# Optimization experiments

Hardware: AMD Instinct MI355X
Metric: run time of the kernel (lower is better)

Reference implementation:

```python
import jax, jax.numpy as jnp
import numpy as np

DIM = 512
HEADS = 8
HEAD_DIM = DIM // HEADS
SCALING = float(np.sqrt(HEAD_DIM))
B, S = 8, 2048


def setup_inputs() -> dict:
    key = jax.random.key(0)
    ks = jax.random.split(key, 6)
    x = jax.random.normal(ks[0], (B, S, DIM), dtype=jnp.float32)
    mask = jax.random.randint(ks[1], (B, S), 0, 2).astype(bool)
    mask = mask.at[:, 0].set(False)  # guarantee at least one unmasked key per row
    lim_qkv = 1.0 / np.sqrt(DIM)
    Wqkv = jax.random.uniform(ks[2], (3 * DIM, DIM), minval=-lim_qkv, maxval=lim_qkv, dtype=jnp.float32)
    bqkv = jax.random.uniform(ks[3], (3 * DIM,), minval=-lim_qkv, maxval=lim_qkv, dtype=jnp.float32)
    Wout = jax.random.uniform(ks[4], (DIM, DIM), minval=-lim_qkv, maxval=lim_qkv, dtype=jnp.float32)
    bout = jax.random.uniform(ks[5], (DIM,), minval=-lim_qkv, maxval=lim_qkv, dtype=jnp.float32)
    ln_g = jnp.ones((DIM,), dtype=jnp.float32)
    ln_b = jnp.zeros((DIM,), dtype=jnp.float32)
    return {"x": x, "mask": mask, "Wqkv": Wqkv, "bqkv": bqkv, "Wout": Wout, "bout": bout, "ln_g": ln_g, "ln_b": ln_b}


def reference(x, mask, Wqkv, bqkv, Wout, bout, ln_g, ln_b):
    b, s, _ = x.shape
    qkv = x @ Wqkv.T + bqkv                                   # [b, s, 3*dim]
    qkv = qkv.reshape(b, s, HEADS, HEAD_DIM, 3)               # torch reshape semantics (interleaved)
    q = qkv[..., 0]                                           # [b, s, h, d]
    k = qkv[..., 1]
    v = jax.nn.elu(qkv[..., 2])
    attn = jnp.einsum('bqhd,bkhd->bhqk', q, k) / SCALING      # [b, h, s, s]
    bias = jnp.where(mask[:, None, None, :], -jnp.inf, 0.0).astype(attn.dtype)
    attn = jax.nn.softmax(attn + bias, axis=-1)
    out = jnp.einsum('bhqk,bkhd->bqhd', attn, v).reshape(b, s, DIM)
    out = out @ Wout.T + bout
    mu = jnp.mean(out, axis=-1, keepdims=True)
    var = jnp.var(out, axis=-1, keepdims=True)
    out = (out - mu) / jnp.sqrt(var + 1e-5) * ln_g + ln_b
    return jax.nn.elu(out)
```

## Files before the change

kernel.cpp:

```cpp
#include <hip/hip_runtime.h>

#define DIM 512
#define HEADS 8
#define HD 64
#define NB 8
#define NS 2048
#define SCALE_INV 0.125f
#define NEG_BIG -1e30f
#define QSZ 8388608

typedef __attribute__((ext_vector_type(8))) short bf16x8;
typedef __attribute__((ext_vector_type(4))) float f32x4;

__device__ __forceinline__ float elu_f(float x) {
    return x > 0.0f ? x : (__expf(x) - 1.0f);
}
__device__ __forceinline__ short f2bf(float x) {
    union { float f; unsigned u; } v; v.f = x;
    unsigned r = v.u + 0x7FFFu + ((v.u >> 16) & 1u);
    return (short)(r >> 16);
}
__device__ __forceinline__ unsigned pack_bf_t(float a, float b) {
    union { float f; unsigned u; } va, vb; va.f = a; vb.f = b;
    return (va.u >> 16) | (vb.u & 0xFFFF0000u);
}

__device__ __forceinline__ void gload16(const void* g, void* l) {
    __builtin_amdgcn_global_load_lds(
        (const __attribute__((address_space(1))) unsigned*)g,
        (__attribute__((address_space(3))) unsigned*)l, 16, 0, 0);
}
__device__ __forceinline__ void gload4(const void* g, void* l) {
    __builtin_amdgcn_global_load_lds(
        (const __attribute__((address_space(1))) unsigned*)g,
        (__attribute__((address_space(3))) unsigned*)l, 4, 0, 0);
}

#define X4 2097152
#define W14 196608
#define W24 65536
__global__ __launch_bounds__(256) void prep(
    const float* __restrict__ x, const float* __restrict__ Wqkv,
    const float* __restrict__ bqkv, const float* __restrict__ Wout,
    const int* __restrict__ mask,
    short* __restrict__ xb, short* __restrict__ Wp,
    float* __restrict__ bp, short* __restrict__ Wob,
    float* __restrict__ maskf)
{
    int i = blockIdx.x * 256 + threadIdx.x;
    if (i < X4) {
        float4 v = *(const float4*)(x + (size_t)i * 4);
        ushort4 o; o.x = (unsigned short)f2bf(v.x); o.y = (unsigned short)f2bf(v.y);
        o.z = (unsigned short)f2bf(v.z); o.w = (unsigned short)f2bf(v.w);
        *(ushort4*)(xb + (size_t)i * 4) = o;
    } else if (i < X4 + W14) {
        int j = i - X4;
        int np = j >> 7, k = (j & 127) * 4;
        int w = np >> 9, h = (np >> 6) & 7, d = np & 63;
        int n = h * 192 + d * 3 + w;
        float4 v = *(const float4*)(Wqkv + (size_t)n * 512 + k);
        ushort4 o; o.x = (unsigned short)f2bf(v.x); o.y = (unsigned short)f2bf(v.y);
        o.z = (unsigned short)f2bf(v.z); o.w = (unsigned short)f2bf(v.w);
        *(ushort4*)(Wp + (size_t)np * 512 + k) = o;
    } else if (i < X4 + W14 + W24) {
        int j = i - X4 - W14;
        float4 v = *(const float4*)(Wout + (size_t)j * 4);
        ushort4 o; o.x = (unsigned short)f2bf(v.x); o.y = (unsigned short)f2bf(v.y);
        o.z = (unsigned short)f2bf(v.z); o.w = (unsigned short)f2bf(v.w);
        *(ushort4*)(Wob + (size_t)j * 4) = o;
    } else if (i < X4 + W14 + W24 + 1536) {
        int j = i - X4 - W14 - W24;
        int w = j >> 9, h = (j >> 6) & 7, d = j & 63;
        bp[j] = bqkv[h * 192 + d * 3 + w];
    } else {
        int j = i - X4 - W14 - W24 - 1536;
        maskf[j] = mask[j] ? NEG_BIG : 0.0f;
    }
}

__global__ __launch_bounds__(256) void qkv_mfma(
    const short* __restrict__ A, const short* __restrict__ Bw,
    const float* __restrict__ bp, short* __restrict__ QKV)
{
    __shared__ short smem[2 * 128 * 64];
    short* As = smem;
    short* Bs = smem + 128 * 64;
    const int t = threadIdx.x, lane = t & 63, wv = t >> 6;
    const int c = lane & 15, quad = lane >> 4;
    const int wr = wv >> 1, wc = wv & 1;
    const int rsub = lane >> 3;
    const int csA = (lane & 7) ^ rsub;
    const int m0 = blockIdx.x * 128, n0 = blockIdx.y * 128;
    f32x4 acc[4][4];
    #pragma unroll
    for (int mi = 0; mi < 4; ++mi)
        #pragma unroll
        for (int nj = 0; nj < 4; ++nj)
            #pragma unroll
            for (int i = 0; i < 4; ++i) acc[mi][nj][i] = 0.0f;

    for (int k0 = 0; k0 < 512; k0 += 64) {
        if (k0) __syncthreads();
        #pragma unroll
        for (int p = 0; p < 4; ++p) {
            int r = p * 32 + wv * 8 + rsub;
            gload16(A  + (size_t)(m0 + r) * 512 + k0 + csA * 8, &As[(p * 4 + wv) * 512]);
            gload16(Bw + (size_t)(n0 + r) * 512 + k0 + csA * 8, &Bs[(p * 4 + wv) * 512]);
        }
        __syncthreads();
        bf16x8 af[4][2], bfr[4][2];
        #pragma unroll
        for (int mi = 0; mi < 4; ++mi) {
            int ar = wr * 64 + mi * 16 + c;
            af[mi][0] = *(const bf16x8*)&As[ar * 64 + ((quad       ^ (ar & 7)) * 8)];
            af[mi][1] = *(const bf16x8*)&As[ar * 64 + (((4 + quad) ^ (ar & 7)) * 8)];
        }
        #pragma unroll
        for (int nj = 0; nj < 4; ++nj) {
            int br = wc * 64 + nj * 16 + c;
            bfr[nj][0] = *(const bf16x8*)&Bs[br * 64 + ((quad       ^ (br & 7)) * 8)];
            bfr[nj][1] = *(const bf16x8*)&Bs[br * 64 + (((4 + quad) ^ (br & 7)) * 8)];
        }
        __builtin_amdgcn_s_setprio(1);
        #pragma unroll
        for (int mi = 0; mi < 4; ++mi)
            #pragma unroll
            for (int nj = 0; nj < 4; ++nj) {
                acc[mi][nj] = __builtin_amdgcn_mfma_f32_16x16x32_bf16(af[mi][0], bfr[nj][0], acc[mi][nj], 0, 0, 0);
                acc[mi][nj] = __builtin_amdgcn_mfma_f32_16x16x32_bf16(af[mi][1], bfr[nj][1], acc[mi][nj], 0, 0, 0);
            }
        __builtin_amdgcn_s_setprio(0);
    }

    const int w  = n0 >> 9;
    const int b  = m0 >> 11;
    const int hh = ((n0 + wc * 64) >> 6) & 7;
    float bv[4];
    #pragma unroll
    for (int nj = 0; nj < 4; ++nj) bv[nj] = bp[n0 + wc * 64 + nj * 16 + c];

    if (w < 2) {
        short* out = QKV + (size_t)w * QSZ + (size_t)(b * 8 + hh) * NS * 64;
        #pragma unroll
        for (int mi = 0; mi < 4; ++mi)
            #pragma unroll
            for (int i = 0; i < 4; ++i) {
                int s = (m0 & (NS - 1)) + wr * 64 + mi * 16 + quad * 4 + i;
                #pragma unroll
                for (int nj = 0; nj < 4; ++nj)
                    out[(size_t)s * 64 + nj * 16 + c] = f2bf(acc[mi][nj][i] + bv[nj]);
            }
    } else {
        __syncthreads();
        short* T = smem;
        #pragma unroll
        for (int mi = 0; mi < 4; ++mi)
            #pragma unroll
            for (int i = 0; i < 4; ++i) {
                int ml = wr * 64 + mi * 16 + quad * 4 + i;
                int mb = ml >> 3, mr = ml & 7;
                #pragma unroll
                for (int nj = 0; nj < 4; ++nj) {
                    int nl = wc * 64 + nj * 16 + c;
                    T[nl * 128 + ((mb ^ (nl & 15)) * 8) + mr] =
                        f2bf(elu_f(acc[mi][nj][i] + bv[nj]));
                }
            }
        __syncthreads();
        short* Vt = QKV + (size_t)2 * QSZ;
        #pragma unroll
        for (int p = 0; p < 8; ++p) {
            int idx = p * 256 + t, row = idx >> 4, ch = idx & 15;
            uint4 v = *(const uint4*)&T[row * 128 + ((ch ^ (row & 15)) * 8)];
            int d = row & 63;
            int h2 = ((n0 + row) >> 6) & 7;
            int sg = (m0 & (NS - 1)) + ch * 8;
            int kt = sg >> 6, ks = sg & 63;
            *(uint4*)(Vt + (((size_t)(b * 8 + h2) * 32 + kt) * 64 + d) * 64 + ks) = v;
        }
    }
}

__global__ __launch_bounds__(512, 6) void attn_mfma(
    const short* __restrict__ Qg, const short* __restrict__ Kg,
    const short* __restrict__ Vg, const float* __restrict__ maskf,
    short* __restrict__ O)
{
    __shared__ short QP[128 * 64];
    __shared__ short Ks[2][64 * 64];
    __shared__ short Vs[2][64 * 64];
    __shared__ float msk[2][64];

    const int t = threadIdx.x;
    const int lane = t & 63;
    const int wv = t >> 6;
    const int c = lane & 15;
    const int quad = lane >> 4;
    const int bid = blockIdx.x;
    const int qt = bid & 15;
    const int h  = (bid >> 4) & 7;
    const int b  = bid >> 7;
    const int g  = b * 8 + h;
    const size_t base = (size_t)g * NS * HD;
    const int q0 = qt * 128;

    const int rsub = lane >> 3;
    const int csA  = (lane & 7) ^ rsub;
    const int csV  = ((lane & 7) - rsub) & 7;

    #pragma unroll
    for (int p = 0; p < 2; ++p) {
        int r = wv * 16 + p * 8 + rsub;
        gload16(Qg + base + (size_t)(q0 + r) * HD + csA * 8, &QP[(wv * 2 + p) * 512]);
    }
    {
        int r = wv * 8 + rsub;
        gload16(Kg + base + (size_t)r * HD + csA * 8, &Ks[0][wv * 512]);
        gload16(Vg + (((size_t)g * 32 + 0) * 64 + r) * 64 + csV * 8, &Vs[0][wv * 512]);
        if (wv == 0) gload4(maskf + (size_t)b * NS + lane, &msk[0][0]);
    }
    __syncthreads();

    const int mq = wv * 16 + c;
    const bf16x8 bq0 = *(const bf16x8*)&QP[mq * 64 + ((quad       ^ (mq & 7)) * 8)];
    const bf16x8 bq1 = *(const bf16x8*)&QP[mq * 64 + (((4 + quad) ^ (mq & 7)) * 8)];

    {
        int r = wv * 8 + rsub;
        gload16(Kg + base + (size_t)(64 + r) * HD + csA * 8, &Ks[1][wv * 512]);
        gload16(Vg + (((size_t)g * 32 + 1) * 64 + r) * 64 + csV * 8, &Vs[1][wv * 512]);
        if (wv == 0) gload4(maskf + (size_t)b * NS + 64 + lane, &msk[1][0]);
    }

    f32x4 o[4];
    #pragma unroll
    for (int dc = 0; dc < 4; ++dc)
        #pragma unroll
        for (int i = 0; i < 4; ++i) o[dc][i] = 0.0f;
    float lp = 0.0f;

    const int prow = wv * 16 + c;
    const int prot = 8 * (c & 7);

    for (int kt = 0; kt < 32; ++kt) {
        const int cur = kt & 1;
        const short* Kc = Ks[cur];
        const short* Vc = Vs[cur];

        f32x4 st[4];
        __builtin_amdgcn_s_setprio(1);
        #pragma unroll
        for (int ks = 0; ks < 4; ++ks) {
            int kr = ks * 16 + c;
            bf16x8 ak0 = *(const bf16x8*)&Kc[kr * 64 + ((quad       ^ (kr & 7)) * 8)];
            bf16x8 ak1 = *(const bf16x8*)&Kc[kr * 64 + (((4 + quad) ^ (kr & 7)) * 8)];
            f32x4 a = {0.0f, 0.0f, 0.0f, 0.0f};
            a = __builtin_amdgcn_mfma_f32_16x16x32_bf16(ak0, bq0, a, 0, 0, 0);
            a = __builtin_amdgcn_mfma_f32_16x16x32_bf16(ak1, bq1, a, 0, 0, 0);
            st[ks] = a;
        }
        __builtin_amdgcn_s_setprio(0);

        #pragma unroll
        for (int ks = 0; ks < 4; ++ks) {
            float4 mb = *(const float4*)&msk[cur][ks * 16 + quad * 4];
            float p0 = __expf(st[ks][0] * SCALE_INV + mb.x);
            float p1 = __expf(st[ks][1] * SCALE_INV + mb.y);
            float p2 = __expf(st[ks][2] * SCALE_INV + mb.z);
            float p3 = __expf(st[ks][3] * SCALE_INV + mb.w);
            lp += (p0 + p1) + (p2 + p3);
            uint2 pk;
            pk.x = pack_bf_t(p0, p1);
            pk.y = pack_bf_t(p2, p3);
            *(uint2*)&QP[prow * 64 + ((ks * 16 + quad * 4 + prot) & 63)] = pk;
        }

        bf16x8 bp0 = *(const bf16x8*)&QP[prow * 64 + ((quad * 8 + prot) & 63)];
        bf16x8 bp1 = *(const bf16x8*)&QP[prow * 64 + ((32 + quad * 8 + prot) & 63)];
        __builtin_amdgcn_s_setprio(1);
        #pragma unroll
        for (int dc = 0; dc < 4; ++dc) {
            int d = dc * 16 + c;
            int vrot = 8 * (d & 7);
            bf16x8 av0 = *(const bf16x8*)&Vc[d * 64 + ((quad * 8 + vrot) & 63)];
            bf16x8 av1 = *(const bf16x8*)&Vc[d * 64 + ((32 + quad * 8 + vrot) & 63)];
            o[dc] = __builtin_amdgcn_mfma_f32_16x16x32_bf16(av0, bp0, o[dc], 0, 0, 0);
            o[dc] = __builtin_amdgcn_mfma_f32_16x16x32_bf16(av1, bp1, o[dc], 0, 0, 0);
        }
        __builtin_amdgcn_s_setprio(0);

        __syncthreads();

        if (kt + 2 < 32) {
            int r = wv * 8 + rsub;
            int k0n = (kt + 2) * 64;
            gload16(Kg + base + (size_t)(k0n + r) * HD + csA * 8, &Ks[cur][wv * 512]);
            gload16(Vg + (((size_t)g * 32 + (kt + 2)) * 64 + r) * 64 + csV * 8, &Vs[cur][wv * 512]);
            if (wv == 0) gload4(maskf + (size_t)b * NS + k0n + lane, &msk[cur][0]);
        }
    }

    lp += __shfl_xor(lp, 16);
    lp += __shfl_xor(lp, 32);
    float inv = 1.0f / lp;

    int q = q0 + wv * 16 + c;
    short* orow = O + ((size_t)(b * NS + q)) * DIM + h * HD + quad * 4;
    #pragma unroll
    for (int dc = 0; dc < 4; ++dc) {
        uint2 pk;
        pk.x = (unsigned)(unsigned short)f2bf(o[dc][0] * inv)
             | ((unsigned)(unsigned short)f2bf(o[dc][1] * inv) << 16);
        pk.y = (unsigned)(unsigned short)f2bf(o[dc][2] * inv)
             | ((unsigned)(unsigned short)f2bf(o[dc][3] * inv) << 16);
        *(uint2*)(orow + dc * 16) = pk;
    }
}

__global__ __launch_bounds__(256) void out_mfma(
    const short* __restrict__ A, const short* __restrict__ Bw,
    const float* __restrict__ bias, float* __restrict__ Z)
{
    __shared__ short smem[2 * 128 * 64];
    short* As = smem;
    short* Bs = smem + 128 * 64;
    const int t = threadIdx.x, lane = t & 63, wv = t >> 6;
    const int c = lane & 15, quad = lane >> 4;
    const int wr = wv >> 1, wc = wv & 1;
    const int rsub = lane >> 3;
    const int csA = (lane & 7) ^ rsub;
    const int m0 = blockIdx.x * 128, n0 = blockIdx.y * 128;
    f32x4 acc[4][4];
    #pragma unroll
    for (int mi = 0; mi < 4; ++mi)
        #pragma unroll
        for (int nj = 0; nj < 4; ++nj)
            #pragma unroll
            for (int i = 0; i < 4; ++i) acc[mi][nj][i] = 0.0f;

    for (int k0 = 0; k0 < 512; k0 += 64) {
        if (k0) __syncthreads();
        #pragma unroll
        for (int p = 0; p < 4; ++p) {
            int r = p * 32 + wv * 8 + rsub;
            gload16(A  + (size_t)(m0 + r) * 512 + k0 + csA * 8, &As[(p * 4 + wv) * 512]);
            gload16(Bw + (size_t)(n0 + r) * 512 + k0 + csA * 8, &Bs[(p * 4 + wv) * 512]);
        }
        __syncthreads();
        bf16x8 af[4][2], bfr[4][2];
        #pragma unroll
        for (int mi = 0; mi < 4; ++mi) {
            int ar = wr * 64 + mi * 16 + c;
            af[mi][0] = *(const bf16x8*)&As[ar * 64 + ((quad       ^ (ar & 7)) * 8)];
            af[mi][1] = *(const bf16x8*)&As[ar * 64 + (((4 + quad) ^ (ar & 7)) * 8)];
        }
        #pragma unroll
        for (int nj = 0; nj < 4; ++nj) {
            int br = wc * 64 + nj * 16 + c;
            bfr[nj][0] = *(const bf16x8*)&Bs[br * 64 + ((quad       ^ (br & 7)) * 8)];
            bfr[nj][1] = *(const bf16x8*)&Bs[br * 64 + (((4 + quad) ^ (br & 7)) * 8)];
        }
        __builtin_amdgcn_s_setprio(1);
        #pragma unroll
        for (int mi = 0; mi < 4; ++mi)
            #pragma unroll
            for (int nj = 0; nj < 4; ++nj) {
                acc[mi][nj] = __builtin_amdgcn_mfma_f32_16x16x32_bf16(af[mi][0], bfr[nj][0], acc[mi][nj], 0, 0, 0);
                acc[mi][nj] = __builtin_amdgcn_mfma_f32_16x16x32_bf16(af[mi][1], bfr[nj][1], acc[mi][nj], 0, 0, 0);
            }
        __builtin_amdgcn_s_setprio(0);
    }
    #pragma unroll
    for (int mi = 0; mi < 4; ++mi)
        #pragma unroll
        for (int i = 0; i < 4; ++i) {
            int mrow = m0 + wr * 64 + mi * 16 + quad * 4 + i;
            #pragma unroll
            for (int nj = 0; nj < 4; ++nj) {
                int n = n0 + wc * 64 + nj * 16 + c;
                Z[(size_t)mrow * 512 + n] = acc[mi][nj][i] + bias[n];
            }
        }
}

__global__ __launch_bounds__(256) void ln_elu(
    const float* __restrict__ Z, const float* __restrict__ g,
    const float* __restrict__ bt, float* __restrict__ out)
{
    const int row = blockIdx.x;
    const float* z = Z + (size_t)row * DIM;
    const int t = threadIdx.x;
    float v0 = z[t], v1 = z[t + 256];
    float s  = v0 + v1;
    float ss = v0 * v0 + v1 * v1;
    #pragma unroll
    for (int off = 32; off > 0; off >>= 1) {
        s  += __shfl_down(s, off);
        ss += __shfl_down(ss, off);
    }
    __shared__ float rs[4], rss[4];
    int wid = t >> 6, lane = t & 63;
    if (lane == 0) { rs[wid] = s; rss[wid] = ss; }
    __syncthreads();
    float S1 = rs[0] + rs[1] + rs[2] + rs[3];
    float S2 = rss[0] + rss[1] + rss[2] + rss[3];
    float mu  = S1 * (1.0f / DIM);
    float var = S2 * (1.0f / DIM) - mu * mu;
    float rstd = rsqrtf(var + 1e-5f);
    float y0 = (v0 - mu) * rstd * g[t]       + bt[t];
    float y1 = (v1 - mu) * rstd * g[t + 256] + bt[t + 256];
    out[(size_t)row * DIM + t]       = elu_f(y0);
    out[(size_t)row * DIM + t + 256] = elu_f(y1);
}

extern "C" void kernel_launch(void* const* d_in, const int* in_sizes, int n_in,
                              void* d_out, int out_size, void* d_ws, size_t ws_size,
                              hipStream_t stream)
{
    const float* x    = (const float*)d_in[0];
    const int*   mask = (const int*)d_in[1];
    const float* Wqkv = (const float*)d_in[2];
    const float* bqkv = (const float*)d_in[3];
    const float* Wout = (const float*)d_in[4];
    const float* bout = (const float*)d_in[5];
    const float* ln_g = (const float*)d_in[6];
    const float* ln_b = (const float*)d_in[7];
    float* out = (float*)d_out;

    short* xb   = (short*)d_ws;
    short* Wp   = xb + QSZ;
    short* Wob  = Wp + 786432;
    short* QKV  = Wob + 262144;
    short* ATTb = QKV + 3 * (size_t)QSZ;
    float* bp   = (float*)(ATTb + QSZ);
    float* Zb   = bp + 1536;
    float* maskf = Zb + (size_t)QSZ - 16384;

    prep<<<9286, 256, 0, stream>>>(x, Wqkv, bqkv, Wout, mask, xb, Wp, bp, Wob, maskf);
    qkv_mfma<<<dim3(128, 12), 256, 0, stream>>>(xb, Wp, bp, QKV);
    attn_mfma<<<1024, 512, 0, stream>>>(QKV, QKV + QSZ, QKV + 2 * (size_t)QSZ, maskf, ATTb);
    out_mfma<<<dim3(128, 4), 256, 0, stream>>>(ATTb, Wob, bout, Zb);
    ln_elu<<<NB * NS, 256, 0, stream>>>(Zb, ln_g, ln_b, out);
}
```

Measured before the change: 253.4 us.

## Split attention KV tile across wave pairs with 32-row query tiles and merge partials

Reorganizes the attention kernel so each wave handles 32 query rows and half of each 64-key tile. Each K/V fragment loaded from LDS now feeds two MFMAs, and the partial outputs are merged through LDS at the end. It also replaces __expf with raw v_exp_f32 on pre-scaled log2 inputs, packs bf16 with the hardware pack instruction, and computes row sums with an MFMA against a ones vector. The costs are more accumulator registers (occupancy hint lowered from 6 to 4), an extra sync, and a final cross-wave reduction, aimed at cutting LDS reads and VALU work per MFMA.

```diff
diff --git a/kernel.cpp b/kernel.cpp
--- a/kernel.cpp
+++ b/kernel.cpp
@@ -6,6 +6,7 @@
 #define NB 8
 #define NS 2048
 #define SCALE_INV 0.125f
+#define C2F 0.18033688011112042f
 #define NEG_BIG -1e30f
 #define QSZ 8388608
 
@@ -20,9 +21,11 @@
     unsigned r = v.u + 0x7FFFu + ((v.u >> 16) & 1u);
     return (short)(r >> 16);
 }
-__device__ __forceinline__ unsigned pack_bf_t(float a, float b) {
-    union { float f; unsigned u; } va, vb; va.f = a; vb.f = b;
-    return (va.u >> 16) | (vb.u & 0xFFFF0000u);
+__device__ __forceinline__ float exp2_hw(float x) {
+    float r; asm("v_exp_f32 %0, %1" : "=v"(r) : "v"(x)); return r;
+}
+__device__ __forceinline__ unsigned cvt_pk_bf16(float a, float b) {
+    unsigned r; asm("v_cvt_pk_bf16_f32 %0, %1, %2" : "=v"(r) : "v"(a), "v"(b)); return r;
 }
 
 __device__ __forceinline__ void gload16(const void* g, void* l) {
@@ -181,19 +184,22 @@
     }
 }
 
-__global__ __launch_bounds__(512, 6) void attn_mfma(
+__global__ __launch_bounds__(512, 4) void attn_mfma(
     const short* __restrict__ Qg, const short* __restrict__ Kg,
     const short* __restrict__ Vg, const float* __restrict__ maskf,
     short* __restrict__ O)
 {
-    __shared__ short QP[128 * 64];
+    __shared__ short Pt[128 * 64];
     __shared__ short Ks[2][64 * 64];
     __shared__ short Vs[2][64 * 64];
     __shared__ float msk[2][64];
+    __shared__ float lw[128];
 
     const int t = threadIdx.x;
     const int lane = t & 63;
     const int wv = t >> 6;
+    const int wq = wv & 3;
+    const int wk = wv >> 2;
     const int c = lane & 15;
     const int quad = lane >> 4;
     const int bid = blockIdx.x;
@@ -211,7 +217,7 @@
     #pragma unroll
     for (int p = 0; p < 2; ++p) {
         int r = wv * 16 + p * 8 + rsub;
-        gload16(Qg + base + (size_t)(q0 + r) * HD + csA * 8, &QP[(wv * 2 + p) * 512]);
+        gload16(Qg + base + (size_t)(q0 + r) * HD + csA * 8, &Pt[(wv * 2 + p) * 512]);
     }
     {
         int r = wv * 8 + rsub;
@@ -221,9 +227,14 @@
     }
     __syncthreads();
 
-    const int mq = wv * 16 + c;
-    const bf16x8 bq0 = *(const bf16x8*)&QP[mq * 64 + ((quad       ^ (mq & 7)) * 8)];
-    const bf16x8 bq1 = *(const bf16x8*)&QP[mq * 64 + (((4 + quad) ^ (mq & 7)) * 8)];
+    bf16x8 bq[2][2];
+    #pragma unroll
+    for (int nj = 0; nj < 2; ++nj) {
+        int mq = wq * 32 + nj * 16 + c;
+        bq[nj][0] = *(const bf16x8*)&Pt[mq * 64 + ((quad       ^ (mq & 7)) * 8)];
+        bq[nj][1] = *(const bf16x8*)&Pt[mq * 64 + (((4 + quad) ^ (mq & 7)) * 8)];
+    }
+    __syncthreads();
 
     {
         int r = wv * 8 + rsub;
@@ -232,60 +243,83 @@
         if (wv == 0) gload4(maskf + (size_t)b * NS + 64 + lane, &msk[1][0]);
     }
 
-    f32x4 o[4];
+    bf16x8 onesA;
+    #pragma unroll
+    for (int i = 0; i < 8; ++i) onesA[i] = (short)0x3F80;
+
+    f32x4 o[4][2];
     #pragma unroll
     for (int dc = 0; dc < 4; ++dc)
         #pragma unroll
-        for (int i = 0; i < 4; ++i) o[dc][i] = 0.0f;
-    float lp = 0.0f;
-
-    const int prow = wv * 16 + c;
-    const int prot = 8 * (c & 7);
+        for (int nj = 0; nj < 2; ++nj)
+            #pragma unroll
+            for (int i = 0; i < 4; ++i) o[dc][nj][i] = 0.0f;
+    f32x4 lacc[2];
+    #pragma unroll
+    for (int nj = 0; nj < 2; ++nj)
+        #pragma unroll
+        for (int i = 0; i < 4; ++i) lacc[nj][i] = 0.0f;
+
+    const int prot  = 8 * (c & 7);
+    const int kbase = wk * 32;
 
     for (int kt = 0; kt < 32; ++kt) {
         const int cur = kt & 1;
         const short* Kc = Ks[cur];
         const short* Vc = Vs[cur];
 
-        f32x4 st[4];
+        f32x4 st[2][2];
         __builtin_amdgcn_s_setprio(1);
         #pragma unroll
-        for (int ks = 0; ks < 4; ++ks) {
-            int kr = ks * 16 + c;
+        for (int ks = 0; ks < 2; ++ks) {
+            int kr = kbase + ks * 16 + c;
             bf16x8 ak0 = *(const bf16x8*)&Kc[kr * 64 + ((quad       ^ (kr & 7)) * 8)];
             bf16x8 ak1 = *(const bf16x8*)&Kc[kr * 64 + (((4 + quad) ^ (kr & 7)) * 8)];
-            f32x4 a = {0.0f, 0.0f, 0.0f, 0.0f};
-            a = __builtin_amdgcn_mfma_f32_16x16x32_bf16(ak0, bq0, a, 0, 0, 0);
-            a = __builtin_amdgcn_mfma_f32_16x16x32_bf16(ak1, bq1, a, 0, 0, 0);
-            st[ks] = a;
+            #pragma unroll
+            for (int nj = 0; nj < 2; ++nj) {
+                f32x4 a = {0.0f, 0.0f, 0.0f, 0.0f};
+                a = __builtin_amdgcn_mfma_f32_16x16x32_bf16(ak0, bq[nj][0], a, 0, 0, 0);
+                a = __builtin_amdgcn_mfma_f32_16x16x32_bf16(ak1, bq[nj][1], a, 0, 0, 0);
+                st[ks][nj] = a;
+            }
         }
         __builtin_amdgcn_s_setprio(0);
 
         #pragma unroll
-        for (int ks = 0; ks < 4; ++ks) {
-            float4 mb = *(const float4*)&msk[cur][ks * 16 + quad * 4];
-            float p0 = __expf(st[ks][0] * SCALE_INV + mb.x);
-            float p1 = __expf(st[ks][1] * SCALE_INV + mb.y);
-            float p2 = __expf(st[ks][2] * SCALE_INV + mb.z);
-            float p3 = __expf(st[ks][3] * SCALE_INV + mb.w);
-            lp += (p0 + p1) + (p2 + p3);
-            uint2 pk;
-            pk.x = pack_bf_t(p0, p1);
-            pk.y = pack_bf_t(p2, p3);
-            *(uint2*)&QP[prow * 64 + ((ks * 16 + quad * 4 + prot) & 63)] = pk;
-        }
-
-        bf16x8 bp0 = *(const bf16x8*)&QP[prow * 64 + ((quad * 8 + prot) & 63)];
-        bf16x8 bp1 = *(const bf16x8*)&QP[prow * 64 + ((32 + quad * 8 + prot) & 63)];
+        for (int ks = 0; ks < 2; ++ks) {
+            float4 mb = *(const float4*)&msk[cur][kbase + ks * 16 + quad * 4];
+            #pragma unroll
+            for (int nj = 0; nj < 2; ++nj) {
+                float p0 = exp2_hw(st[ks][nj][0] * C2F + mb.x);
+                float p1 = exp2_hw(st[ks][nj][1] * C2F + mb.y);
+                float p2 = exp2_hw(st[ks][nj][2] * C2F + mb.z);
+                float p3 = exp2_hw(st[ks][nj][3] * C2F + mb.w);
+                uint2 pk;
+                pk.x = cvt_pk_bf16(p0, p1);
+                pk.y = cvt_pk_bf16(p2, p3);
+                *(uint2*)&Pt[(wq * 32 + nj * 16 + c) * 64 +
+                             ((kbase + ks * 16 + quad * 4 + prot) & 63)] = pk;
+            }
+        }
+
+        bf16x8 bp[2];
+        #pragma unroll
+        for (int nj = 0; nj < 2; ++nj)
+            bp[nj] = *(const bf16x8*)&Pt[(wq * 32 + nj * 16 + c) * 64 +
+                                         ((kbase + quad * 8 + prot) & 63)];
+
         __builtin_amdgcn_s_setprio(1);
+        #pragma unroll
+        for (int nj = 0; nj < 2; ++nj)
+            lacc[nj] = __builtin_amdgcn_mfma_f32_16x16x32_bf16(onesA, bp[nj], lacc[nj], 0, 0, 0);
         #pragma unroll
         for (int dc = 0; dc < 4; ++dc) {
             int d = dc * 16 + c;
             int vrot = 8 * (d & 7);
-            bf16x8 av0 = *(const bf16x8*)&Vc[d * 64 + ((quad * 8 + vrot) & 63)];
-            bf16x8 av1 = *(const bf16x8*)&Vc[d * 64 + ((32 + quad * 8 + vrot) & 63)];
-            o[dc] = __builtin_amdgcn_mfma_f32_16x16x32_bf16(av0, bp0, o[dc], 0, 0, 0);
-            o[dc] = __builtin_amdgcn_mfma_f32_16x16x32_bf16(av1, bp1, o[dc], 0, 0, 0);
+            bf16x8 av = *(const bf16x8*)&Vc[d * 64 + ((kbase + quad * 8 + vrot) & 63)];
+            #pragma unroll
+            for (int nj = 0; nj < 2; ++nj)
+                o[dc][nj] = __builtin_amdgcn_mfma_f32_16x16x32_bf16(av, bp[nj], o[dc][nj], 0, 0, 0);
         }
         __builtin_amdgcn_s_setprio(0);
 
@@ -300,20 +334,45 @@
         }
     }
 
-    lp += __shfl_xor(lp, 16);
-    lp += __shfl_xor(lp, 32);
-    float inv = 1.0f / lp;
-
-    int q = q0 + wv * 16 + c;
-    short* orow = O + ((size_t)(b * NS + q)) * DIM + h * HD + quad * 4;
-    #pragma unroll
-    for (int dc = 0; dc < 4; ++dc) {
-        uint2 pk;
-        pk.x = (unsigned)(unsigned short)f2bf(o[dc][0] * inv)
-             | ((unsigned)(unsigned short)f2bf(o[dc][1] * inv) << 16);
-        pk.y = (unsigned)(unsigned short)f2bf(o[dc][2] * inv)
-             | ((unsigned)(unsigned short)f2bf(o[dc][3] * inv) << 16);
-        *(uint2*)(orow + dc * 16) = pk;
+    float* rb = ((wq < 2) ? (float*)&Ks[0][0] : (float*)&Vs[0][0])
+                + (wq & 1) * 2048 + lane * 32;
+    if (wk == 1) {
+        #pragma unroll
+        for (int dc = 0; dc < 4; ++dc)
+            #pragma unroll
+            for (int nj = 0; nj < 2; ++nj)
+                *(f32x4*)&rb[(((dc << 1) | nj) ^ (lane & 7)) << 2] = o[dc][nj];
+        if (quad == 0) {
+            lw[wq * 32 + c]      = lacc[0][0];
+            lw[wq * 32 + 16 + c] = lacc[1][0];
+        }
+    }
+    __syncthreads();
+    if (wk == 0) {
+        float l0 = lacc[0][0] + lw[wq * 32 + c];
+        float l1 = lacc[1][0] + lw[wq * 32 + 16 + c];
+        float inv0 = 1.0f / l0;
+        float inv1 = 1.0f / l1;
+        #pragma unroll
+        for (int dc = 0; dc < 4; ++dc)
+            #pragma unroll
+            for (int nj = 0; nj < 2; ++nj)
+                o[dc][nj] += *(const f32x4*)&rb[(((dc << 1) | nj) ^ (lane & 7)) << 2];
+        #pragma unroll
+        for (int nj = 0; nj < 2; ++nj) {
+            float inv = nj ? inv1 : inv0;
+            int q = q0 + wq * 32 + nj * 16 + c;
+            short* orow = O + ((size_t)(b * NS + q)) * DIM + h * HD + quad * 4;
+            #pragma unroll
+            for (int dc = 0; dc < 4; ++dc) {
+                uint2 pk;
+                pk.x = (unsigned)(unsigned short)f2bf(o[dc][nj][0] * inv)
+                     | ((unsigned)(unsigned short)f2bf(o[dc][nj][1] * inv) << 16);
+                pk.y = (unsigned)(unsigned short)f2bf(o[dc][nj][2] * inv)
+                     | ((unsigned)(unsigned short)f2bf(o[dc][nj][3] * inv) << 16);
+                *(uint2*)(orow + dc * 16) = pk;
+            }
+        }
     }
 }
 
```

After: 238.6 us. 1.06x faster.
